# Kernel tuning notes

Measured on AMD Instinct MI355X. Metric: run time of the kernel, lower is better.

Reference implementation:

```python
import jax, jax.numpy as jnp
import numpy as np

NUM_GROUPS = 32
EPS = 1e-6


def group_norm(x, gamma, beta):
    # x: [B, C, H, W]
    B, C, H, W = x.shape
    xg = x.reshape(B, NUM_GROUPS, C // NUM_GROUPS, H, W)
    mean = jnp.mean(xg, axis=(2, 3, 4), keepdims=True)
    var = jnp.var(xg, axis=(2, 3, 4), keepdims=True)
    xn = ((xg - mean) * jax.lax.rsqrt(var + EPS)).reshape(B, C, H, W)
    return xn * gamma[None, :, None, None] + beta[None, :, None, None]


def conv1x1(x, w, b):
    # x: [B, C, H, W], w: [O, C], b: [O]  (1x1 conv == channel matmul)
    return jnp.einsum('oc,bchw->bohw', w, x) + b[None, :, None, None]


def setup_inputs() -> dict:
    key = jax.random.key(0)
    ks = jax.random.split(key, 10)
    B, C, H, W = 16, 512, 32, 32
    s = 1.0 / np.sqrt(C)
    inp = {
        'hidden_states': jax.random.normal(ks[0], (B, C, H, W), dtype=jnp.float32),
        'norm_gamma': jnp.ones((C,), dtype=jnp.float32),
        'norm_beta': jnp.zeros((C,), dtype=jnp.float32),
        'wq': jax.random.normal(ks[1], (C, C), dtype=jnp.float32) * s,
        'bq': jnp.zeros((C,), dtype=jnp.float32),
        'wk': jax.random.normal(ks[2], (C, C), dtype=jnp.float32) * s,
        'bk': jnp.zeros((C,), dtype=jnp.float32),
        'wv': jax.random.normal(ks[3], (C, C), dtype=jnp.float32) * s,
        'bv': jnp.zeros((C,), dtype=jnp.float32),
        'wo': jax.random.normal(ks[4], (C, C), dtype=jnp.float32) * s,
        'bo': jnp.zeros((C,), dtype=jnp.float32),
    }
    return inp


def reference(hidden_states, norm_gamma, norm_beta, wq, bq, wk, bk, wv, bv, wo, bo):
    residual = hidden_states
    h = group_norm(hidden_states, norm_gamma, norm_beta)
    q = conv1x1(h, wq, bq)  # [B, C, H, W]
    k = conv1x1(h, wk, bk)
    v = conv1x1(h, wv, bv)
    B, C, H, W = q.shape
    N = H * W
    qf = q.reshape(B, C, N)  # [B, C, N]
    kf = k.reshape(B, C, N)
    vf = v.reshape(B, C, N)
    scale = float(C) ** (-0.5)
    # attn_weights[b, i, j] = sum_c q[b,c,i] * k[b,c,j]
    attn = jnp.einsum('bci,bcj->bij', qf, kf) * scale
    attn = jax.nn.softmax(attn, axis=2)
    # out[b, c, i] = sum_j v[b,c,j] * attn[b,i,j]
    out = jnp.einsum('bcj,bij->bci', vf, attn).reshape(B, C, H, W)
    out = conv1x1(out, wo, bo)
    return residual + out
```

## Files before the change

### kernel.cpp

```cpp
#include <hip/hip_runtime.h>

typedef __attribute__((ext_vector_type(4))) float f32x4;
typedef __attribute__((ext_vector_type(8))) __bf16 bf16x8;
typedef __attribute__((ext_vector_type(4))) unsigned short us4;
typedef __attribute__((ext_vector_type(8))) unsigned short us8;

#define B_  16
#define C_  512
#define N_  1024
#define G_  32
#define GS  16

__device__ inline unsigned short f2bf(float f) {
  unsigned u = __builtin_bit_cast(unsigned, f);
  u += 0x7fffu + ((u >> 16) & 1u);
  return (unsigned short)(u >> 16);
}

#define GLOAD_LDS16(gp, lp) __builtin_amdgcn_global_load_lds( \
    (const __attribute__((address_space(1))) unsigned int*)(gp), \
    (__attribute__((address_space(3))) unsigned int*)(lp), 16, 0, 0)

__global__ __launch_bounds__(256) void gn_fused(const float* __restrict__ x,
                                                const float* __restrict__ gamma,
                                                const float* __restrict__ beta,
                                                unsigned short* __restrict__ ht) {
  int bg = blockIdx.x;
  int b = bg >> 5, g = bg & 31;
  int tid = threadIdx.x;
  __shared__ float Lx[16][1028];
  __shared__ float r1[256], r2[256];
  const float* xp = x + ((long)b * C_ + g * 16) * N_;
  float s = 0.f, ss = 0.f;
#pragma unroll
  for (int i = 0; i < 16; ++i) {
    f32x4 v = *(const f32x4*)&xp[(long)i * N_ + tid * 4];
    s  += v.x + v.y + v.z + v.w;
    ss += v.x * v.x + v.y * v.y + v.z * v.z + v.w * v.w;
    *(f32x4*)&Lx[i][tid * 4] = v;
  }
  r1[tid] = s; r2[tid] = ss; __syncthreads();
  for (int off = 128; off > 0; off >>= 1) {
    if (tid < off) { r1[tid] += r1[tid + off]; r2[tid] += r2[tid + off]; }
    __syncthreads();
  }
  float mean = r1[0] * (1.f / 16384.f);
  float var  = r2[0] * (1.f / 16384.f) - mean * mean;
  float rstd = rsqrtf(var + 1e-6f);
  float gm[8], bt[8];
  int cbase = g * 16 + (tid & 1) * 8;
#pragma unroll
  for (int k = 0; k < 8; ++k) {
    gm[k] = gamma[cbase + k] * rstd;
    bt[k] = beta[cbase + k] - mean * gm[k];
  }
#pragma unroll
  for (int j = 0; j < 8; ++j) {
    int lin = tid + j * 256;
    int n = lin >> 1;
    int c8 = (lin & 1) * 8;
    us8 o;
#pragma unroll
    for (int k = 0; k < 8; ++k)
      o[k] = f2bf(Lx[c8 + k][n] * gm[k] + bt[k]);
    *(us8*)&ht[((long)b * N_ + n) * C_ + g * 16 + c8] = o;
  }
}

__global__ __launch_bounds__(256) void convert_w(const float* __restrict__ wq, const float* __restrict__ wk,
                                                 const float* __restrict__ wo,
                                                 const float* __restrict__ bq, const float* __restrict__ bk,
                                                 const float* __restrict__ bv,
                                                 unsigned short* __restrict__ wqk,
                                                 unsigned short* __restrict__ wob, float* __restrict__ bqk,
                                                 float* __restrict__ bvo) {
  long bid = blockIdx.x;
  int tid = threadIdx.x;
  long i = bid * 256 + tid;
  if (i < C_ * C_) {
    wqk[i]           = f2bf(wq[i]);
    wqk[C_ * C_ + i] = f2bf(wk[i]);
    wob[i]           = f2bf(wo[i]);
  }
  if (i < C_) { bqk[i] = bq[i]; bqk[C_ + i] = bk[i]; }
  if (bid >= 1024) {
    int o = (int)(bid - 1024) * 256 + tid;
    const float* wr = wo + (long)o * 512;
    float acc = 0.f;
    for (int c = 0; c < 512; c += 4) {
      f32x4 w4 = *(const f32x4*)&wr[c];
      f32x4 b4 = *(const f32x4*)&bv[c];
      acc += w4.x * b4.x + w4.y * b4.y + w4.z * b4.z + w4.w * b4.w;
    }
    bvo[o] = acc;
  }
}

__global__ __launch_bounds__(256) void transpose_wv(const float* __restrict__ wv,
                                                    unsigned short* __restrict__ wvT) {
  int c0 = blockIdx.x * 64, k0 = blockIdx.y * 64;
  int tid = threadIdx.x;
  __shared__ float Lt[64][65];
#pragma unroll
  for (int i = 0; i < 4; ++i) {
    int lin = tid + i * 256;
    int rr = lin >> 4;
    int q4 = (lin & 15) * 4;
    f32x4 v = *(const f32x4*)&wv[(long)(c0 + rr) * 512 + k0 + q4];
    Lt[q4 + 0][rr] = v.x; Lt[q4 + 1][rr] = v.y;
    Lt[q4 + 2][rr] = v.z; Lt[q4 + 3][rr] = v.w;
  }
  __syncthreads();
#pragma unroll
  for (int i = 0; i < 2; ++i) {
    int lin = tid + i * 256;
    int kk = lin >> 3;
    int cc = (lin & 7) * 8;
    us8 o;
#pragma unroll
    for (int j = 0; j < 8; ++j) o[j] = f2bf(Lt[kk][cc + j]);
    *(us8*)&wvT[(long)(k0 + kk) * 512 + c0 + cc] = o;
  }
}

__device__ inline f32x4 mfma16(bf16x8 a, bf16x8 b, f32x4 c) {
  return __builtin_amdgcn_mfma_f32_16x16x32_bf16(a, b, c, 0, 0, 0);
}

__global__ __launch_bounds__(256) void wprod(const unsigned short* __restrict__ wob,
                                             const unsigned short* __restrict__ wvT,
                                             unsigned short* __restrict__ WVO) {
  int row0 = blockIdx.x * 64, col0 = blockIdx.y * 64;
  int tid = threadIdx.x, lane = tid & 63, w = tid >> 6;
  int lr = lane & 15, kh = (lane >> 4) * 8;
  f32x4 acc4[4];
#pragma unroll
  for (int n = 0; n < 4; ++n) acc4[n] = f32x4{0.f, 0.f, 0.f, 0.f};
  for (int k0 = 0; k0 < 512; k0 += 32) {
    bf16x8 af = *(const bf16x8*)&wob[(long)(row0 + w * 16 + lr) * 512 + k0 + kh];
#pragma unroll
    for (int n = 0; n < 4; ++n) {
      bf16x8 bf8 = *(const bf16x8*)&wvT[(long)(col0 + n * 16 + lr) * 512 + k0 + kh];
      acc4[n] = mfma16(af, bf8, acc4[n]);
    }
  }
  int rb = (lane >> 4) * 4;
#pragma unroll
  for (int n = 0; n < 4; ++n)
#pragma unroll
    for (int r = 0; r < 4; ++r)
      WVO[(long)(row0 + w * 16 + rb + r) * 512 + col0 + n * 16 + lr] = f2bf(acc4[n][r]);
}

__device__ inline int swz(int b) { return b ^ (((b >> 9) & 1) << 5); }

template<int EPI, int SHX, int SHY, int XSWZ>
__global__ __launch_bounds__(256, 2) void gemm128(
    const unsigned short* __restrict__ A, long lda, long Az,
    const unsigned short* __restrict__ Bm, long ldb, long Bz,
    void* __restrict__ Dp, long ldd, long Dz,
    const float* __restrict__ bias, float scale, int K,
    const float* __restrict__ residual, float* __restrict__ rs) {
  int bx = blockIdx.x, by = blockIdx.y, bz = blockIdx.z;
  if constexpr (XSWZ) {
    int lin = bx + ((by + (bz << SHY)) << SHX);
    int cpx = 1 << (SHX + SHY + 4 - 3);
    int l2  = (lin & 7) * cpx + (lin >> 3);
    bx = l2 & ((1 << SHX) - 1);
    by = (l2 >> SHX) & ((1 << SHY) - 1);
    bz = l2 >> (SHX + SHY);
  }
  const int z = bz;
  const long row0 = (long)bx * 128;
  const long col0 = (long)by * 128;
  const int tid  = threadIdx.x;
  const int lane = tid & 63;
  const int wave = tid >> 6;
  const int wm = wave >> 1;
  const int wn = wave & 1;
  const int lr = lane & 15;
  const int khb = (lane >> 4) * 16;

  __shared__ unsigned short Abuf[2][8192];
  __shared__ unsigned short Bbuf[2][8192];
  __shared__ float sred[128];

  const unsigned short* Ab = A  + (long)z * Az;
  const unsigned short* Bb = Bm + (long)z * Bz;

  if constexpr (EPI == 7) {
    if (tid < 128) {
      const float* rp = rs + ((long)z * 1024 + row0 + tid) * 16;
      float s = 0.f;
#pragma unroll
      for (int i = 0; i < 16; ++i) s += rp[i];
      sred[tid] = 1.f / s;
    }
    asm volatile("s_waitcnt lgkmcnt(0)" ::: "memory");
  }

  const unsigned short* gA[4];
  const unsigned short* gB[4];
#pragma unroll
  for (int r = 0; r < 4; ++r) {
    int L = swz(r * 4096 + tid * 16);
    gA[r] = Ab + (row0 + (L >> 7)) * lda + ((L & 127) >> 1);
    gB[r] = Bb + (col0 + (L >> 7)) * ldb + ((L & 127) >> 1);
  }

  f32x4 acc[4][4];
#pragma unroll
  for (int m = 0; m < 4; ++m)
#pragma unroll
    for (int n = 0; n < 4; ++n) acc[m][n] = f32x4{0.f, 0.f, 0.f, 0.f};

  const int NT = K >> 6;
  const int ldsO = wave * 512;

#pragma unroll
  for (int r = 0; r < 4; ++r) {
    GLOAD_LDS16(gA[r], &Abuf[0][r * 2048 + ldsO]);
    GLOAD_LDS16(gB[r], &Bbuf[0][r * 2048 + ldsO]);
  }

  for (int t = 0; t < NT; ++t) {
    int tn = t + 1; if (tn == NT) tn = 0;
    const long ko = (long)tn << 6;
    const int nb = (t + 1) & 1;
#pragma unroll
    for (int r = 0; r < 4; ++r) {
      GLOAD_LDS16(gA[r] + ko, &Abuf[nb][r * 2048 + ldsO]);
      GLOAD_LDS16(gB[r] + ko, &Bbuf[nb][r * 2048 + ldsO]);
    }
    asm volatile("s_waitcnt vmcnt(8)" ::: "memory");
    __builtin_amdgcn_s_barrier();
    __builtin_amdgcn_sched_barrier(0);
    const unsigned short* Al = Abuf[t & 1];
    const unsigned short* Bl = Bbuf[t & 1];
#pragma unroll
    for (int kk = 0; kk < 2; ++kk) {
      bf16x8 af[4], bfr[4];
#pragma unroll
      for (int m = 0; m < 4; ++m) {
        int Pb = swz((wm * 64 + m * 16 + lr) * 128 + kk * 64 + khb);
        af[m] = *(const bf16x8*)((const char*)Al + Pb);
      }
#pragma unroll
      for (int n = 0; n < 4; ++n) {
        int Pb = swz((wn * 64 + n * 16 + lr) * 128 + kk * 64 + khb);
        bfr[n] = *(const bf16x8*)((const char*)Bl + Pb);
      }
      __builtin_amdgcn_s_setprio(1);
#pragma unroll
      for (int m = 0; m < 4; ++m)
#pragma unroll
        for (int n = 0; n < 4; ++n)
          acc[m][n] = mfma16(af[m], bfr[n], acc[m][n]);
      __builtin_amdgcn_s_setprio(0);
    }
    __builtin_amdgcn_sched_barrier(0);
    __builtin_amdgcn_s_barrier();
    __builtin_amdgcn_sched_barrier(0);
  }
  asm volatile("s_waitcnt vmcnt(0)" ::: "memory");
  __builtin_amdgcn_s_barrier();

  const int rb = (lane >> 4) * 4;

  if constexpr (EPI == 7) {
#pragma unroll
    for (int m = 0; m < 4; ++m) {
      int lrow = wm * 64 + m * 16 + rb;
      long gr0 = row0 + lrow;
#pragma unroll
      for (int n = 0; n < 4; ++n) {
        long gc = col0 + wn * 64 + n * 16 + lr;
        long o = (long)z * (512L * 1024L) + gc * 1024L + gr0;
        f32x4 res = *(const f32x4*)&residual[o];
        float bb = bias[gc];
        f32x4 st;
#pragma unroll
        for (int r = 0; r < 4; ++r)
          st[r] = acc[m][n][r] * sred[lrow + r] + bb + res[r];
        *(f32x4*)&((float*)Dp)[o] = st;
      }
    }
    return;
  }

  float* slab = ((float*)(void*)Abuf) + wave * 1088;
  const int jt = by;
  unsigned short* Dst = (unsigned short*)Dp + (long)z * Dz;
#pragma unroll
  for (int m = 0; m < 4; ++m) {
    float ps[4] = {0.f, 0.f, 0.f, 0.f};
#pragma unroll
    for (int n = 0; n < 4; ++n) {
      float bcol = 0.f;
      if constexpr (EPI == 0) bcol = bias[col0 + wn * 64 + n * 16 + lr];
#pragma unroll
      for (int r = 0; r < 4; ++r) {
        float v = acc[m][n][r];
        if constexpr (EPI == 0) v += bcol;
        else if constexpr (EPI == 1) v += bias[row0 + wm * 64 + m * 16 + rb + r];
        else if constexpr (EPI == 5) { v = exp2f(v * scale); ps[r] += v; }
        slab[(rb + r) * 68 + n * 16 + lr] = v;
      }
    }
    if constexpr (EPI == 5) {
#pragma unroll
      for (int r = 0; r < 4; ++r) {
        ps[r] += __shfl_xor(ps[r], 1);
        ps[r] += __shfl_xor(ps[r], 2);
        ps[r] += __shfl_xor(ps[r], 4);
        ps[r] += __shfl_xor(ps[r], 8);
      }
      if (lr == 0) {
#pragma unroll
        for (int r = 0; r < 4; ++r)
          rs[((long)z * 1024 + row0 + wm * 64 + m * 16 + rb + r) * 16 + jt * 2 + wn] = ps[r];
      }
    }
#pragma unroll
    for (int p = 0; p < 2; ++p) {
      int rl = p * 8 + (lane >> 3);
      int c8 = (lane & 7) * 8;
      f32x4 v0 = *(const f32x4*)&slab[rl * 68 + c8];
      f32x4 v1 = *(const f32x4*)&slab[rl * 68 + c8 + 4];
      us8 o;
      o[0] = f2bf(v0.x); o[1] = f2bf(v0.y); o[2] = f2bf(v0.z); o[3] = f2bf(v0.w);
      o[4] = f2bf(v1.x); o[5] = f2bf(v1.y); o[6] = f2bf(v1.z); o[7] = f2bf(v1.w);
      *(us8*)&Dst[(row0 + wm * 64 + m * 16 + rl) * ldd + col0 + wn * 64 + c8] = o;
    }
  }
}

extern "C" void kernel_launch(void* const* d_in, const int* in_sizes, int n_in,
                              void* d_out, int out_size, void* d_ws, size_t ws_size,
                              hipStream_t stream) {
  const float* x     = (const float*)d_in[0];
  const float* gamma = (const float*)d_in[1];
  const float* beta  = (const float*)d_in[2];
  const float* wq    = (const float*)d_in[3];
  const float* bq    = (const float*)d_in[4];
  const float* wk    = (const float*)d_in[5];
  const float* bk    = (const float*)d_in[6];
  const float* wv    = (const float*)d_in[7];
  const float* bv    = (const float*)d_in[8];
  const float* wo    = (const float*)d_in[9];
  const float* bo    = (const float*)d_in[10];
  float* out = (float*)d_out;

  char* ws = (char*)d_ws;
  unsigned short* ht   = (unsigned short*)(ws + 0);
  unsigned short* qkt  = (unsigned short*)(ws + 16777216);
  unsigned short* VWT  = (unsigned short*)(ws + 50331648);
  unsigned short* S    = (unsigned short*)(ws + 83886080);
  unsigned short* wqkb = (unsigned short*)(ws + 117440512);
  unsigned short* wvT  = (unsigned short*)(ws + 119537664);
  unsigned short* wob  = (unsigned short*)(ws + 120061952);
  unsigned short* WVO  = (unsigned short*)(ws + 120586240);
  float* bqk           = (float*)(ws + 121110528);
  float* bvo           = (float*)(ws + 121114624);
  float* rs            = (float*)(ws + 121122816);

  convert_w<<<1026, 256, 0, stream>>>(wq, wk, wo, bq, bk, bv,
                                      wqkb, wob, bqk, bvo);
  transpose_wv<<<dim3(8, 8), 256, 0, stream>>>(wv, wvT);
  wprod<<<dim3(8, 8), 256, 0, stream>>>(wob, wvT, WVO);
  gn_fused<<<512, 256, 0, stream>>>(x, gamma, beta, ht);

  gemm128<0, 0, 0, 0><<<dim3(128, 8, 1), 256, 0, stream>>>(ht, 512, 0, wqkb, 512, 0,
                                                           qkt, 1024, 0, bqk, 0.f, 512, nullptr, nullptr);
  gemm128<1, 0, 0, 0><<<dim3(4, 128, 1), 256, 0, stream>>>(WVO, 512, 0, ht, 512, 0,
                                                           VWT, 16384, 0, bvo, 0.f, 512, nullptr, nullptr);
  gemm128<5, 3, 3, 1><<<dim3(8, 8, 16), 256, 0, stream>>>(qkt, 1024, 1048576L, qkt + 512, 1024, 1048576L,
                                                          S, 1024, 1048576L, nullptr,
                                                          0.06375871416f, 512, nullptr, rs);
  gemm128<7, 3, 2, 1><<<dim3(8, 4, 16), 256, 0, stream>>>(S, 1024, 1048576L,
                                                          VWT, 16384, 1024,
                                                          out, 0, 0, bo, 0.f, 1024, x, rs);
}
```

Before: 147.6 us.

## Make each GEMM block compute two column tiles with a continuous load pipeline

Each gemm block now processes two adjacent 128-wide output column tiles in sequence, with the K-loop running across both. The global-to-LDS prefetch of the second tile overlaps the first tile's epilogue, and the grid is halved. The LDS-staged vectorized bf16 store epilogue is replaced by direct scalar 2-byte stores, which may hurt write coalescing. Halving the grid also reduces parallelism: the attention GEMMs drop to 512 and 256 blocks.

```diff
diff --git a/kernel.cpp b/kernel.cpp
--- a/kernel.cpp
+++ b/kernel.cpp
@@ -155,7 +155,7 @@
 __device__ inline int swz(int b) { return b ^ (((b >> 9) & 1) << 5); }
 
 template<int EPI, int SHX, int SHY, int XSWZ>
-__global__ __launch_bounds__(256, 2) void gemm128(
+__global__ __launch_bounds__(256, 2) void gemm128t(
     const unsigned short* __restrict__ A, long lda, long Az,
     const unsigned short* __restrict__ Bm, long ldb, long Bz,
     void* __restrict__ Dp, long ldd, long Dz,
@@ -172,7 +172,6 @@
   }
   const int z = bz;
   const long row0 = (long)bx * 128;
-  const long col0 = (long)by * 128;
   const int tid  = threadIdx.x;
   const int lane = tid & 63;
   const int wave = tid >> 6;
@@ -200,12 +199,14 @@
   }
 
   const unsigned short* gA[4];
-  const unsigned short* gB[4];
+  const unsigned short* gB[2][4];
 #pragma unroll
   for (int r = 0; r < 4; ++r) {
     int L = swz(r * 4096 + tid * 16);
     gA[r] = Ab + (row0 + (L >> 7)) * lda + ((L & 127) >> 1);
-    gB[r] = Bb + (col0 + (L >> 7)) * ldb + ((L & 127) >> 1);
+#pragma unroll
+    for (int tt = 0; tt < 2; ++tt)
+      gB[tt][r] = Bb + ((long)(by * 2 + tt) * 128 + (L >> 7)) * ldb + ((L & 127) >> 1);
   }
 
   f32x4 acc[4][4];
@@ -214,29 +215,32 @@
 #pragma unroll
     for (int n = 0; n < 4; ++n) acc[m][n] = f32x4{0.f, 0.f, 0.f, 0.f};
 
-  const int NT = K >> 6;
+  const int NT  = K >> 6;
+  const int TOT = NT * 2;
   const int ldsO = wave * 512;
+  const int rb = (lane >> 4) * 4;
 
 #pragma unroll
   for (int r = 0; r < 4; ++r) {
     GLOAD_LDS16(gA[r], &Abuf[0][r * 2048 + ldsO]);
-    GLOAD_LDS16(gB[r], &Bbuf[0][r * 2048 + ldsO]);
-  }
-
-  for (int t = 0; t < NT; ++t) {
-    int tn = t + 1; if (tn == NT) tn = 0;
-    const long ko = (long)tn << 6;
-    const int nb = (t + 1) & 1;
+    GLOAD_LDS16(gB[0][r], &Bbuf[0][r * 2048 + ldsO]);
+  }
+
+  for (int it = 0; it < TOT; ++it) {
+    int s = it + 1; if (s == TOT) s = 0;
+    const int tn = (s >= NT) ? 1 : 0;
+    const long ko = (long)(s - tn * NT) << 6;
+    const int nb = (it + 1) & 1;
 #pragma unroll
     for (int r = 0; r < 4; ++r) {
       GLOAD_LDS16(gA[r] + ko, &Abuf[nb][r * 2048 + ldsO]);
-      GLOAD_LDS16(gB[r] + ko, &Bbuf[nb][r * 2048 + ldsO]);
+      GLOAD_LDS16(gB[tn][r] + ko, &Bbuf[nb][r * 2048 + ldsO]);
     }
     asm volatile("s_waitcnt vmcnt(8)" ::: "memory");
     __builtin_amdgcn_s_barrier();
     __builtin_amdgcn_sched_barrier(0);
-    const unsigned short* Al = Abuf[t & 1];
-    const unsigned short* Bl = Bbuf[t & 1];
+    const unsigned short* Al = Abuf[it & 1];
+    const unsigned short* Bl = Bbuf[it & 1];
 #pragma unroll
     for (int kk = 0; kk < 2; ++kk) {
       bf16x8 af[4], bfr[4];
@@ -259,80 +263,75 @@
       __builtin_amdgcn_s_setprio(0);
     }
     __builtin_amdgcn_sched_barrier(0);
+
+    if ((it & (NT - 1)) == NT - 1) {
+      const int tt = (it >= NT) ? 1 : 0;
+      const long col0 = (long)(by * 2 + tt) * 128;
+      if constexpr (EPI == 7) {
+#pragma unroll
+        for (int m = 0; m < 4; ++m) {
+          int lrow = wm * 64 + m * 16 + rb;
+          long gr0 = row0 + lrow;
+#pragma unroll
+          for (int n = 0; n < 4; ++n) {
+            long gc = col0 + wn * 64 + n * 16 + lr;
+            long o = (long)z * (512L * 1024L) + gc * 1024L + gr0;
+            f32x4 res = *(const f32x4*)&residual[o];
+            float bb = bias[gc];
+            f32x4 st;
+#pragma unroll
+            for (int r = 0; r < 4; ++r)
+              st[r] = acc[m][n][r] * sred[lrow + r] + bb + res[r];
+            *(f32x4*)&((float*)Dp)[o] = st;
+          }
+        }
+      } else {
+        unsigned short* Dst = (unsigned short*)Dp + (long)z * Dz;
+        const int jt = by * 2 + tt;
+#pragma unroll
+        for (int m = 0; m < 4; ++m) {
+          float ps[4] = {0.f, 0.f, 0.f, 0.f};
+#pragma unroll
+          for (int n = 0; n < 4; ++n) {
+            float bcol = 0.f;
+            if constexpr (EPI == 0) bcol = bias[col0 + wn * 64 + n * 16 + lr];
+#pragma unroll
+            for (int r = 0; r < 4; ++r) {
+              long gr = row0 + wm * 64 + m * 16 + rb + r;
+              long gc = col0 + wn * 64 + n * 16 + lr;
+              float v = acc[m][n][r];
+              if constexpr (EPI == 0) v += bcol;
+              else if constexpr (EPI == 1) v += bias[gr];
+              else if constexpr (EPI == 5) { v = exp2f(v * scale); ps[r] += v; }
+              Dst[gr * ldd + gc] = f2bf(v);
+            }
+          }
+          if constexpr (EPI == 5) {
+#pragma unroll
+            for (int r = 0; r < 4; ++r) {
+              ps[r] += __shfl_xor(ps[r], 1);
+              ps[r] += __shfl_xor(ps[r], 2);
+              ps[r] += __shfl_xor(ps[r], 4);
+              ps[r] += __shfl_xor(ps[r], 8);
+            }
+            if (lr == 0) {
+#pragma unroll
+              for (int r = 0; r < 4; ++r)
+                rs[((long)z * 1024 + row0 + wm * 64 + m * 16 + rb + r) * 16 + jt * 2 + wn] = ps[r];
+            }
+          }
+        }
+      }
+#pragma unroll
+      for (int m = 0; m < 4; ++m)
+#pragma unroll
+        for (int n = 0; n < 4; ++n) acc[m][n] = f32x4{0.f, 0.f, 0.f, 0.f};
+    }
+
     __builtin_amdgcn_s_barrier();
     __builtin_amdgcn_sched_barrier(0);
   }
   asm volatile("s_waitcnt vmcnt(0)" ::: "memory");
-  __builtin_amdgcn_s_barrier();
-
-  const int rb = (lane >> 4) * 4;
-
-  if constexpr (EPI == 7) {
-#pragma unroll
-    for (int m = 0; m < 4; ++m) {
-      int lrow = wm * 64 + m * 16 + rb;
-      long gr0 = row0 + lrow;
-#pragma unroll
-      for (int n = 0; n < 4; ++n) {
-        long gc = col0 + wn * 64 + n * 16 + lr;
-        long o = (long)z * (512L * 1024L) + gc * 1024L + gr0;
-        f32x4 res = *(const f32x4*)&residual[o];
-        float bb = bias[gc];
-        f32x4 st;
-#pragma unroll
-        for (int r = 0; r < 4; ++r)
-          st[r] = acc[m][n][r] * sred[lrow + r] + bb + res[r];
-        *(f32x4*)&((float*)Dp)[o] = st;
-      }
-    }
-    return;
-  }
-
-  float* slab = ((float*)(void*)Abuf) + wave * 1088;
-  const int jt = by;
-  unsigned short* Dst = (unsigned short*)Dp + (long)z * Dz;
-#pragma unroll
-  for (int m = 0; m < 4; ++m) {
-    float ps[4] = {0.f, 0.f, 0.f, 0.f};
-#pragma unroll
-    for (int n = 0; n < 4; ++n) {
-      float bcol = 0.f;
-      if constexpr (EPI == 0) bcol = bias[col0 + wn * 64 + n * 16 + lr];
-#pragma unroll
-      for (int r = 0; r < 4; ++r) {
-        float v = acc[m][n][r];
-        if constexpr (EPI == 0) v += bcol;
-        else if constexpr (EPI == 1) v += bias[row0 + wm * 64 + m * 16 + rb + r];
-        else if constexpr (EPI == 5) { v = exp2f(v * scale); ps[r] += v; }
-        slab[(rb + r) * 68 + n * 16 + lr] = v;
-      }
-    }
-    if constexpr (EPI == 5) {
-#pragma unroll
-      for (int r = 0; r < 4; ++r) {
-        ps[r] += __shfl_xor(ps[r], 1);
-        ps[r] += __shfl_xor(ps[r], 2);
-        ps[r] += __shfl_xor(ps[r], 4);
-        ps[r] += __shfl_xor(ps[r], 8);
-      }
-      if (lr == 0) {
-#pragma unroll
-        for (int r = 0; r < 4; ++r)
-          rs[((long)z * 1024 + row0 + wm * 64 + m * 16 + rb + r) * 16 + jt * 2 + wn] = ps[r];
-      }
-    }
-#pragma unroll
-    for (int p = 0; p < 2; ++p) {
-      int rl = p * 8 + (lane >> 3);
-      int c8 = (lane & 7) * 8;
-      f32x4 v0 = *(const f32x4*)&slab[rl * 68 + c8];
-      f32x4 v1 = *(const f32x4*)&slab[rl * 68 + c8 + 4];
-      us8 o;
-      o[0] = f2bf(v0.x); o[1] = f2bf(v0.y); o[2] = f2bf(v0.z); o[3] = f2bf(v0.w);
-      o[4] = f2bf(v1.x); o[5] = f2bf(v1.y); o[6] = f2bf(v1.z); o[7] = f2bf(v1.w);
-      *(us8*)&Dst[(row0 + wm * 64 + m * 16 + rl) * ldd + col0 + wn * 64 + c8] = o;
-    }
-  }
 }
 
 extern "C" void kernel_launch(void* const* d_in, const int* in_sizes, int n_in,
@@ -370,14 +369,14 @@
   wprod<<<dim3(8, 8), 256, 0, stream>>>(wob, wvT, WVO);
   gn_fused<<<512, 256, 0, stream>>>(x, gamma, beta, ht);
 
-  gemm128<0, 0, 0, 0><<<dim3(128, 8, 1), 256, 0, stream>>>(ht, 512, 0, wqkb, 512, 0,
-                                                           qkt, 1024, 0, bqk, 0.f, 512, nullptr, nullptr);
-  gemm128<1, 0, 0, 0><<<dim3(4, 128, 1), 256, 0, stream>>>(WVO, 512, 0, ht, 512, 0,
+  gemm128t<0, 0, 0, 0><<<dim3(128, 4, 1), 256, 0, stream>>>(ht, 512, 0, wqkb, 512, 0,
+                                                            qkt, 1024, 0, bqk, 0.f, 512, nullptr, nullptr);
+  gemm128t<1, 0, 0, 0><<<dim3(4, 64, 1), 256, 0, stream>>>(WVO, 512, 0, ht, 512, 0,
                                                            VWT, 16384, 0, bvo, 0.f, 512, nullptr, nullptr);
-  gemm128<5, 3, 3, 1><<<dim3(8, 8, 16), 256, 0, stream>>>(qkt, 1024, 1048576L, qkt + 512, 1024, 1048576L,
-                                                          S, 1024, 1048576L, nullptr,
-                                                          0.06375871416f, 512, nullptr, rs);
-  gemm128<7, 3, 2, 1><<<dim3(8, 4, 16), 256, 0, stream>>>(S, 1024, 1048576L,
-                                                          VWT, 16384, 1024,
-                                                          out, 0, 0, bo, 0.f, 1024, x, rs);
-}
+  gemm128t<5, 3, 2, 1><<<dim3(8, 4, 16), 256, 0, stream>>>(qkt, 1024, 1048576L, qkt + 512, 1024, 1048576L,
+                                                           S, 1024, 1048576L, nullptr,
+                                                           0.06375871416f, 512, nullptr, rs);
+  gemm128t<7, 3, 1, 1><<<dim3(8, 2, 16), 256, 0, stream>>>(S, 1024, 1048576L,
+                                                           VWT, 16384, 1024,
+                                                           out, 0, 0, bo, 0.f, 1024, x, rs);
+}
```

After: 168.9 us. 14.4% more time.
